# Performance work log

Hardware: AMD Instinct MI355X
Metric: run time of the kernel (lower is better)

Reference implementation:

```python
import jax, jax.numpy as jnp
import numpy as np

B, T, D, H = 8, 1024, 512, 8
D4 = 4 * D
SIGMA = 16.0
EPS = 1e-5


def layer_norm(x, w, b):
    m = jnp.mean(x, axis=-1, keepdims=True)
    v = jnp.mean((x - m) ** 2, axis=-1, keepdims=True)
    return (x - m) * jax.lax.rsqrt(v + EPS) * w + b


def setup_inputs() -> dict:
    key = jax.random.key(0)
    ks = jax.random.split(key, 12)
    return {
        "x": jax.random.normal(ks[0], (B, T, D), jnp.float32),
        "posv": jax.random.randint(ks[1], (B, T), 0, 64, jnp.int32),
        "posh": jax.random.randint(ks[2], (B, T), 0, 64, jnp.int32),
        "norm1_w": jnp.ones((D,), jnp.float32),
        "norm1_b": jnp.zeros((D,), jnp.float32),
        "in_w": jax.random.normal(ks[3], (3 * D, D), jnp.float32) * (D ** -0.5),
        "in_b": jnp.zeros((3 * D,), jnp.float32),
        "out_w": jax.random.normal(ks[4], (D, D), jnp.float32) * (D ** -0.5),
        "out_b": jnp.zeros((D,), jnp.float32),
        "norm2_w": jnp.ones((D,), jnp.float32),
        "norm2_b": jnp.zeros((D,), jnp.float32),
        "w1": jax.random.normal(ks[5], (D4, D), jnp.float32) * (D ** -0.5),
        "b1": jnp.zeros((D4,), jnp.float32),
        "w2": jax.random.normal(ks[6], (D, D4), jnp.float32) * (D4 ** -0.5),
        "b2": jnp.zeros((D,), jnp.float32),
        "gate": jnp.array(0.0, jnp.float32),
    }


def reference(x, posv, posh, norm1_w, norm1_b, in_w, in_b, out_w, out_b,
              norm2_w, norm2_b, w1, b1, w2, b2, gate):
    hd = D // H
    residual = x
    xn = layer_norm(x, norm1_w, norm1_b)

    # --- standard multi-head self-attention (dropout=eval identity) ---
    qkv = xn @ in_w.T + in_b                       # [B,T,3D]
    q, k, v = jnp.split(qkv, 3, axis=-1)
    q = q.reshape(B, T, H, hd).transpose(0, 2, 1, 3)  # [B,H,T,hd]
    k = k.reshape(B, T, H, hd).transpose(0, 2, 1, 3)
    v = v.reshape(B, T, H, hd).transpose(0, 2, 1, 3)
    scores = jnp.einsum("bhqd,bhkd->bhqk", q, k) * (hd ** -0.5)
    attn = jax.nn.softmax(scores, axis=-1)
    ctx = jnp.einsum("bhqk,bhkd->bhqd", attn, v)   # [B,H,T,hd]
    ctx = ctx.transpose(0, 2, 1, 3).reshape(B, T, D)
    std_out = ctx @ out_w.T + out_b

    # --- Gaussian kernel position attention ---
    pos = jnp.stack([posv, posh], axis=-1).astype(jnp.float32)  # [B,T,2]
    dist_sq = jnp.sum((pos[:, :, None, :] - pos[:, None, :, :]) ** 2, axis=-1)  # [B,T,T]
    kw = jnp.exp(-dist_sq / (2.0 * SIGMA ** 2))
    kw = kw / jnp.sum(kw, axis=-1, keepdims=True)
    kernel_out = kw @ xn                            # [B,T,D]

    g = jax.nn.sigmoid(gate)
    x1 = residual + g * std_out + (1.0 - g) * kernel_out

    # --- MLP block ---
    xn2 = layer_norm(x1, norm2_w, norm2_b)
    h = jax.nn.gelu(xn2 @ w1.T + b1, approximate=False)
    return x1 + h @ w2.T + b2
```

## Files before the change

### kernel.cpp

```cpp
#include <hip/hip_runtime.h>
#include <hip/hip_bf16.h>
#include <math.h>

typedef unsigned short ushort_t;
typedef short short8 __attribute__((ext_vector_type(8)));
typedef float f32x4 __attribute__((ext_vector_type(4)));

__device__ __forceinline__ float b2f(ushort_t u) {
  union { unsigned u; float f; } v; v.u = ((unsigned)u) << 16; return v.f;
}
__device__ __forceinline__ ushort_t f2b(float f) {
  union { float f; unsigned u; } v; v.f = f;
  unsigned r = (v.u + 0x7FFFu + ((v.u >> 16) & 1u)) >> 16;
  return (ushort_t)r;
}
__device__ __forceinline__ float gelu_fast(float v) {
  float u = 0.7978845608f * (v + 0.044715f * v * v * v);
  float a = fabsf(u);
  float t = exp2f(a * -2.8853900817779268f);
  float th = (1.f - t) / (1.f + t);
  th = copysignf(th, u);
  return 0.5f * v * (1.f + th);
}

union U16x8 { uint4 v; ushort_t s[8]; };

typedef const __attribute__((address_space(1))) unsigned int glb_u32;
typedef __attribute__((address_space(3))) unsigned int lds_u32;
__device__ __forceinline__ void gl_lds16(const ushort_t* g, ushort_t* l) {
  __builtin_amdgcn_global_load_lds((glb_u32*)g, (lds_u32*)l, 16, 0, 0);
}

__global__ __launch_bounds__(256) void cvt4_kernel(const float* __restrict__ s0,
                                                   const float* __restrict__ s1,
                                                   const float* __restrict__ s2,
                                                   const float* __restrict__ s3,
                                                   ushort_t* __restrict__ d0,
                                                   ushort_t* __restrict__ d1,
                                                   ushort_t* __restrict__ d2,
                                                   ushort_t* __restrict__ d3) {
  long i = (long)blockIdx.x * 256 + threadIdx.x;
  const float* s; ushort_t* d; long off;
  if (i < 196608)       { s = s0; d = d0; off = i; }
  else if (i < 262144)  { s = s1; d = d1; off = i - 196608; }
  else if (i < 524288)  { s = s2; d = d2; off = i - 262144; }
  else                  { s = s3; d = d3; off = i - 524288; }
  float4 f = *(const float4*)(s + off * 4);
  union { uint2 v; ushort_t s[4]; } o;
  o.s[0] = f2b(f.x); o.s[1] = f2b(f.y); o.s[2] = f2b(f.z); o.s[3] = f2b(f.w);
  *(uint2*)(d + off * 4) = o.v;
}

__global__ __launch_bounds__(256) void ln_kernel(const float* __restrict__ x,
                                                 const float* __restrict__ w,
                                                 const float* __restrict__ b,
                                                 ushort_t* __restrict__ out) {
  int tid = threadIdx.x, wave = tid >> 6, lane = tid & 63;
  long token = (long)blockIdx.x * 4 + wave;
  const float* xr = x + token * 512 + lane * 8;
  float4 a0 = *(const float4*)xr;
  float4 a1 = *(const float4*)(xr + 4);
  float xf[8] = {a0.x, a0.y, a0.z, a0.w, a1.x, a1.y, a1.z, a1.w};
  float s = 0.f, sq = 0.f;
#pragma unroll
  for (int i = 0; i < 8; i++) { s += xf[i]; sq += xf[i] * xf[i]; }
#pragma unroll
  for (int off = 1; off < 64; off <<= 1) { s += __shfl_xor(s, off); sq += __shfl_xor(sq, off); }
  float m = s * (1.f / 512.f);
  float var = sq * (1.f / 512.f) - m * m;
  float rs = rsqrtf(var + 1e-5f);
  float4 w0 = *(const float4*)(w + lane * 8);
  float4 w1v = *(const float4*)(w + lane * 8 + 4);
  float4 b0 = *(const float4*)(b + lane * 8);
  float4 b1v = *(const float4*)(b + lane * 8 + 4);
  float wf[8] = {w0.x, w0.y, w0.z, w0.w, w1v.x, w1v.y, w1v.z, w1v.w};
  float bf[8] = {b0.x, b0.y, b0.z, b0.w, b1v.x, b1v.y, b1v.z, b1v.w};
  U16x8 o;
#pragma unroll
  for (int i = 0; i < 8; i++) o.s[i] = f2b((xf[i] - m) * rs * wf[i] + bf[i]);
  *(uint4*)(out + token * 512 + lane * 8) = o.v;
}

__global__ __launch_bounds__(256) void ln_b_kernel(const ushort_t* __restrict__ x,
                                                   const float* __restrict__ w,
                                                   const float* __restrict__ b,
                                                   ushort_t* __restrict__ out) {
  int tid = threadIdx.x, wave = tid >> 6, lane = tid & 63;
  long token = (long)blockIdx.x * 4 + wave;
  U16x8 ux; ux.v = *(const uint4*)(x + token * 512 + lane * 8);
  float xf[8], s = 0.f, sq = 0.f;
#pragma unroll
  for (int i = 0; i < 8; i++) { xf[i] = b2f(ux.s[i]); s += xf[i]; sq += xf[i] * xf[i]; }
#pragma unroll
  for (int off = 1; off < 64; off <<= 1) { s += __shfl_xor(s, off); sq += __shfl_xor(sq, off); }
  float m = s * (1.f / 512.f);
  float var = sq * (1.f / 512.f) - m * m;
  float rs = rsqrtf(var + 1e-5f);
  float4 w0 = *(const float4*)(w + lane * 8);
  float4 w1v = *(const float4*)(w + lane * 8 + 4);
  float4 b0 = *(const float4*)(b + lane * 8);
  float4 b1v = *(const float4*)(b + lane * 8 + 4);
  float wf[8] = {w0.x, w0.y, w0.z, w0.w, w1v.x, w1v.y, w1v.z, w1v.w};
  float bf[8] = {b0.x, b0.y, b0.z, b0.w, b1v.x, b1v.y, b1v.z, b1v.w};
  U16x8 o;
#pragma unroll
  for (int i = 0; i < 8; i++) o.s[i] = f2b((xf[i] - m) * rs * wf[i] + bf[i]);
  *(uint4*)(out + token * 512 + lane * 8) = o.v;
}

__global__ __launch_bounds__(256) void kw_kernel(const int* __restrict__ posv,
                                                 const int* __restrict__ posh,
                                                 ushort_t* __restrict__ kw) {
  int b = blockIdx.x >> 10, i = blockIdx.x & 1023;
  int tid = threadIdx.x;
  const int* pv = posv + b * 1024;
  const int* ph = posh + b * 1024;
  int pvi = pv[i], phi = ph[i];
  int j0 = tid * 4;
  int4 vj = *(const int4*)(pv + j0);
  int4 hj = *(const int4*)(ph + j0);
  int vv[4] = {vj.x, vj.y, vj.z, vj.w};
  int hh[4] = {hj.x, hj.y, hj.z, hj.w};
  float e[4]; float loc = 0.f;
#pragma unroll
  for (int u = 0; u < 4; u++) {
    int dv = pvi - vv[u], dh = phi - hh[u];
    e[u] = expf((float)(dv * dv + dh * dh) * (-1.f / 512.f));
    loc += e[u];
  }
#pragma unroll
  for (int off = 1; off < 64; off <<= 1) loc += __shfl_xor(loc, off);
  __shared__ float wsum[4];
  __shared__ float tot;
  if ((tid & 63) == 0) wsum[tid >> 6] = loc;
  __syncthreads();
  if (tid == 0) tot = wsum[0] + wsum[1] + wsum[2] + wsum[3];
  __syncthreads();
  float inv = 1.f / tot;
  union { uint2 v; ushort_t s[4]; } o;
#pragma unroll
  for (int u = 0; u < 4; u++) o.s[u] = f2b(e[u] * inv);
  *(uint2*)&kw[((long)(b * 1024 + i)) * 1024 + j0] = o.v;
}

__global__ __launch_bounds__(256) void tr_kernel(const ushort_t* __restrict__ in,
                                                 ushort_t* __restrict__ out,
                                                 int R, int C) {
  __shared__ ushort_t tile[64 * 64];
  int z = blockIdx.z, r0 = blockIdx.y * 64, c0 = blockIdx.x * 64;
  const ushort_t* src = in + (long)z * R * C;
  ushort_t* dst = out + (long)z * R * C;
  int tid = threadIdx.x;
  int tr = tid >> 2;
  const ushort_t* s = src + (long)(r0 + tr) * C + c0;
  int g = (tr + (tr >> 4)) & 7;
#pragma unroll
  for (int u = 0; u < 2; u++) {
    int c = (tid & 3) + u * 4;
    *(uint4*)&tile[tr * 64 + (c ^ g) * 8] = *(const uint4*)(s + c * 8);
  }
  __syncthreads();
  int oc = tid >> 2, ob = (tid & 3) * 16;
  U16x8 o0, o1;
#pragma unroll
  for (int j = 0; j < 16; j++) {
    int r = ob + j;
    int gg = (r + (r >> 4)) & 7;
    ushort_t val = tile[r * 64 + (((oc >> 3) ^ gg)) * 8 + (oc & 7)];
    if (j < 8) o0.s[j] = val; else o1.s[j - 8] = val;
  }
  ushort_t* d = dst + (long)(c0 + oc) * R + r0 + ob;
  *(uint4*)d = o0.v;
  *(uint4*)(d + 8) = o1.v;
}

struct GemmP {
  const ushort_t* A; const ushort_t* Bm;
  long sA, sB, sC;
  int lda, ldb, ldc, K;
  const float* biasf;
  const float* residf;
  const ushort_t* auxb;
  const float* auxf;
  float* outf;
  ushort_t* outb;
  ushort_t* qp; ushort_t* kp; ushort_t* vp;
  const float* gate;
};

template <int BM, int BN, int EPI>
__global__ __launch_bounds__(256) void gemm_k(GemmP p) {
  constexpr int TI = BM / 32, TJ = BN / 32;
  constexpr int RA = BM / 64, RB = BN / 64;
  __shared__ ushort_t As[4][BM * 32];
  __shared__ ushort_t Bs[4][BN * 32];
  int tid = threadIdx.x, wv = tid >> 6, lane = tid & 63;
  int quad = lane >> 4, l15 = lane & 15;
  int bl = blockIdx.x + gridDim.x * blockIdx.y;
  int m0 = (bl % gridDim.y) * BM;
  int n0 = (bl / gridDim.y) * BN;
  int z = blockIdx.z;
  const ushort_t* A = p.A + (long)z * p.sA;
  const ushort_t* Bm = p.Bm + (long)z * p.sB;
  int wm = (wv & 1) * (BM / 2), wn = (wv >> 1) * (BN / 2);
  f32x4 acc[TI][TJ];
#pragma unroll
  for (int i = 0; i < TI; i++)
#pragma unroll
    for (int j = 0; j < TJ; j++)
#pragma unroll
      for (int r = 0; r < 4; r++) acc[i][j][r] = 0.f;

  int srow = tid >> 2;
  int sc = ((tid & 3) ^ ((tid >> 3) & 3)) * 8;
  const ushort_t* ga = A + (long)(m0 + srow) * p.lda + sc;
  const ushort_t* gb = Bm + (long)(n0 + srow) * p.ldb + sc;
  long a64 = (long)64 * p.lda, b64 = (long)64 * p.ldb;
  int aswz = (quad ^ ((l15 >> 1) & 3)) * 8;
  int nsteps = p.K >> 5;

#pragma unroll
  for (int s = 0; s < 2; s++) {
#pragma unroll
    for (int rr = 0; rr < RA; rr++)
      gl_lds16(ga + s * 32 + rr * a64, As[s] + rr * 2048 + wv * 512);
#pragma unroll
    for (int rr = 0; rr < RB; rr++)
      gl_lds16(gb + s * 32 + rr * b64, Bs[s] + rr * 2048 + wv * 512);
  }
  __syncthreads();

  for (int ks = 0; ks < nsteps; ks += 2) {
    if (ks + 2 < nsteps) {
#pragma unroll
      for (int s = 0; s < 2; s++) {
        int st = ks + 2 + s, bf = st & 3;
        const ushort_t* a0 = ga + st * 32;
        const ushort_t* b0 = gb + st * 32;
#pragma unroll
        for (int rr = 0; rr < RA; rr++)
          gl_lds16(a0 + rr * a64, As[bf] + rr * 2048 + wv * 512);
#pragma unroll
        for (int rr = 0; rr < RB; rr++)
          gl_lds16(b0 + rr * b64, Bs[bf] + rr * 2048 + wv * 512);
      }
    }
#pragma unroll
    for (int hs = 0; hs < 2; hs++) {
      int cur = (ks + hs) & 3;
      short8 av[TI], bv[TJ];
#pragma unroll
      for (int ti = 0; ti < TI; ti++)
        av[ti] = *(const short8*)&As[cur][(wm + ti * 16 + l15) * 32 + aswz];
#pragma unroll
      for (int tj = 0; tj < TJ; tj++)
        bv[tj] = *(const short8*)&Bs[cur][(wn + tj * 16 + l15) * 32 + aswz];
#pragma unroll
      for (int ti = 0; ti < TI; ti++)
#pragma unroll
        for (int tj = 0; tj < TJ; tj++)
          acc[ti][tj] = __builtin_amdgcn_mfma_f32_16x16x32_bf16(av[ti], bv[tj], acc[ti][tj], 0, 0, 0);
    }
    __syncthreads();
  }

  float g = 0.f;
  if constexpr (EPI == 2) g = 1.f / (1.f + expf(-p.gate[0]));
#pragma unroll
  for (int ti = 0; ti < TI; ti++) {
#pragma unroll
    for (int tj = 0; tj < TJ; tj++) {
#pragma unroll
      for (int r = 0; r < 4; r++) {
        int gm = m0 + wm + ti * 16 + quad * 4 + r;
        int n = n0 + wn + tj * 16 + l15;
        float v = acc[ti][tj][r];
        if constexpr (EPI == 0) {
          v += p.biasf[n];
          int bb = gm >> 10, tt = gm & 1023;
          if (n < 512) {
            int h = n >> 6, d = n & 63;
            p.qp[((long)(bb * 8 + h) * 1024 + tt) * 64 + d] = f2b(v * 0.18033688011112042f);
          } else if (n < 1024) {
            int n2 = n - 512, h = n2 >> 6, d = n2 & 63;
            p.kp[((long)(bb * 8 + h) * 1024 + tt) * 64 + d] = f2b(v);
          } else {
            int n2 = n - 1024, h = n2 >> 6, d = n2 & 63;
            p.vp[((long)(bb * 8 + h) * 1024 + tt) * 64 + d] = f2b(v);
          }
        } else if constexpr (EPI == 1) {
          p.outb[(long)z * p.sC + (long)gm * p.ldc + n] = f2b(v);
        } else if constexpr (EPI == 2) {
          v += p.biasf[n];
          long idx = (long)gm * 512 + n;
          p.outb[idx] = f2b(p.residf[idx] + g * v + (1.f - g) * b2f(p.auxb[idx]));
        } else if constexpr (EPI == 3) {
          v += p.biasf[n];
          p.outb[(long)gm * p.ldc + n] = f2b(gelu_fast(v));
        } else {
          v += p.biasf[n];
          long idx = (long)gm * 512 + n;
          p.outf[idx] = v + b2f(p.auxb[idx]);
        }
      }
    }
  }
}

template <int EPI>
__global__ __launch_bounds__(512, 2) void gemm256_k(GemmP p) {
  __shared__ __align__(16) ushort_t As[2][256 * 64];
  __shared__ __align__(16) ushort_t Bs[2][256 * 64];
  int tid = threadIdx.x, wv = tid >> 6, lane = tid & 63;
  int quad = lane >> 4, l15 = lane & 15;
  int m0 = blockIdx.x * 256, n0 = blockIdx.y * 256;
  int wr = wv >> 2, wc = wv & 3;

  int srow = tid >> 3;
  int scol = ((tid & 7) ^ (srow & 7)) * 8;
  const ushort_t* ga = p.A + (long)(m0 + srow) * p.lda + scol;
  const ushort_t* gb = p.Bm + (long)(n0 + srow) * p.ldb + scol;
  long a64 = (long)64 * p.lda, b64 = (long)64 * p.ldb;
  int NT = p.K >> 6;

  f32x4 acc[8][4];
#pragma unroll
  for (int i = 0; i < 8; i++)
#pragma unroll
    for (int j = 0; j < 4; j++)
#pragma unroll
      for (int r = 0; r < 4; r++) acc[i][j][r] = 0.f;

  gl_lds16(gb + 0 * b64, Bs[0] + 0 * 4096 + wv * 512);
  gl_lds16(gb + 1 * b64, Bs[0] + 1 * 4096 + wv * 512);
  gl_lds16(gb + 2 * b64, Bs[0] + 2 * 4096 + wv * 512);
  gl_lds16(gb + 3 * b64, Bs[0] + 3 * 4096 + wv * 512);
  gl_lds16(ga + 0 * a64, As[0] + 0 * 4096 + wv * 512);
  gl_lds16(ga + 2 * a64, As[0] + 2 * 4096 + wv * 512);
  gl_lds16(ga + 1 * a64, As[0] + 1 * 4096 + wv * 512);
  gl_lds16(ga + 3 * a64, As[0] + 3 * 4096 + wv * 512);
  asm volatile("s_waitcnt vmcnt(2)" ::: "memory");
  __builtin_amdgcn_s_barrier();

  int c0 = (quad ^ (l15 & 7)) * 8;
  int c1 = ((quad + 4) ^ (l15 & 7)) * 8;

  for (int t = 0; t < NT; t++) {
    int bt = t & 1, nx = bt ^ 1;
    bool pre = (t + 1 < NT);
    const ushort_t* Ab = &As[bt][(wr * 128 + l15) * 64];
    const ushort_t* Bb = &Bs[bt][(wc * 64 + l15) * 64];
    const ushort_t* gak = ga + (t + 1) * 64;
    const ushort_t* gbk = gb + (t + 1) * 64;
    short8 a[8], bn0[4], bn1[4];

#pragma unroll
    for (int mf = 0; mf < 4; mf++) {
      a[2 * mf]     = *(const short8*)(Ab + mf * 1024 + c0);
      a[2 * mf + 1] = *(const short8*)(Ab + mf * 1024 + c1);
    }
#pragma unroll
    for (int nf = 0; nf < 2; nf++) {
      bn0[2 * nf]     = *(const short8*)(Bb + nf * 1024 + c0);
      bn0[2 * nf + 1] = *(const short8*)(Bb + nf * 1024 + c1);
    }
    if (pre) {
      gl_lds16(gbk + 0 * b64, Bs[nx] + 0 * 4096 + wv * 512);
      gl_lds16(gbk + 1 * b64, Bs[nx] + 1 * 4096 + wv * 512);
    }
    __builtin_amdgcn_s_barrier();
    __builtin_amdgcn_s_setprio(1);
#pragma unroll
    for (int mf = 0; mf < 4; mf++)
#pragma unroll
      for (int nf = 0; nf < 2; nf++) {
        acc[mf][nf] = __builtin_amdgcn_mfma_f32_16x16x32_bf16(a[2 * mf], bn0[2 * nf], acc[mf][nf], 0, 0, 0);
        acc[mf][nf] = __builtin_amdgcn_mfma_f32_16x16x32_bf16(a[2 * mf + 1], bn0[2 * nf + 1], acc[mf][nf], 0, 0, 0);
      }
    __builtin_amdgcn_s_setprio(0);
    __builtin_amdgcn_s_barrier();

#pragma unroll
    for (int nf = 0; nf < 2; nf++) {
      bn1[2 * nf]     = *(const short8*)(Bb + (2 + nf) * 1024 + c0);
      bn1[2 * nf + 1] = *(const short8*)(Bb + (2 + nf) * 1024 + c1);
    }
    if (pre) {
      gl_lds16(gbk + 2 * b64, Bs[nx] + 2 * 4096 + wv * 512);
      gl_lds16(gbk + 3 * b64, Bs[nx] + 3 * 4096 + wv * 512);
    }
    __builtin_amdgcn_s_barrier();
    __builtin_amdgcn_s_setprio(1);
#pragma unroll
    for (int mf = 0; mf < 4; mf++)
#pragma unroll
      for (int nf = 0; nf < 2; nf++) {
        acc[mf][2 + nf] = __builtin_amdgcn_mfma_f32_16x16x32_bf16(a[2 * mf], bn1[2 * nf], acc[mf][2 + nf], 0, 0, 0);
        acc[mf][2 + nf] = __builtin_amdgcn_mfma_f32_16x16x32_bf16(a[2 * mf + 1], bn1[2 * nf + 1], acc[mf][2 + nf], 0, 0, 0);
      }
    __builtin_amdgcn_s_setprio(0);
    if (pre) asm volatile("s_waitcnt vmcnt(4)" ::: "memory");
    else     asm volatile("s_waitcnt vmcnt(0)" ::: "memory");
    __builtin_amdgcn_s_barrier();

#pragma unroll
    for (int mf = 0; mf < 4; mf++) {
      a[2 * mf]     = *(const short8*)(Ab + (4 + mf) * 1024 + c0);
      a[2 * mf + 1] = *(const short8*)(Ab + (4 + mf) * 1024 + c1);
    }
    if (pre) {
      gl_lds16(gak + 0 * a64, As[nx] + 0 * 4096 + wv * 512);
      gl_lds16(gak + 2 * a64, As[nx] + 2 * 4096 + wv * 512);
    }
    __builtin_amdgcn_s_barrier();
    __builtin_amdgcn_s_setprio(1);
#pragma unroll
    for (int mf = 0; mf < 4; mf++)
#pragma unroll
      for (int nf = 0; nf < 2; nf++) {
        acc[4 + mf][2 + nf] = __builtin_amdgcn_mfma_f32_16x16x32_bf16(a[2 * mf], bn1[2 * nf], acc[4 + mf][2 + nf], 0, 0, 0);
        acc[4 + mf][2 + nf] = __builtin_amdgcn_mfma_f32_16x16x32_bf16(a[2 * mf + 1], bn1[2 * nf + 1], acc[4 + mf][2 + nf], 0, 0, 0);
      }
    __builtin_amdgcn_s_setprio(0);
    __builtin_amdgcn_s_barrier();

    if (pre) {
      gl_lds16(gak + 1 * a64, As[nx] + 1 * 4096 + wv * 512);
      gl_lds16(gak + 3 * a64, As[nx] + 3 * 4096 + wv * 512);
    }
    __builtin_amdgcn_s_barrier();
    __builtin_amdgcn_s_setprio(1);
#pragma unroll
    for (int mf = 0; mf < 4; mf++)
#pragma unroll
      for (int nf = 0; nf < 2; nf++) {
        acc[4 + mf][nf] = __builtin_amdgcn_mfma_f32_16x16x32_bf16(a[2 * mf], bn0[2 * nf], acc[4 + mf][nf], 0, 0, 0);
        acc[4 + mf][nf] = __builtin_amdgcn_mfma_f32_16x16x32_bf16(a[2 * mf + 1], bn0[2 * nf + 1], acc[4 + mf][nf], 0, 0, 0);
      }
    __builtin_amdgcn_s_setprio(0);
    if (pre) asm volatile("s_waitcnt vmcnt(2)" ::: "memory");
    __builtin_amdgcn_s_barrier();
  }

#pragma unroll
  for (int mf = 0; mf < 8; mf++) {
#pragma unroll
    for (int nf = 0; nf < 4; nf++) {
#pragma unroll
      for (int r = 0; r < 4; r++) {
        int gm = m0 + wr * 128 + mf * 16 + quad * 4 + r;
        int n = n0 + wc * 64 + nf * 16 + l15;
        float v = acc[mf][nf][r];
        if constexpr (EPI == 0) {
          v += p.biasf[n];
          int bb = gm >> 10, tt = gm & 1023;
          if (n < 512) {
            int h = n >> 6, d = n & 63;
            p.qp[((long)(bb * 8 + h) * 1024 + tt) * 64 + d] = f2b(v * 0.18033688011112042f);
          } else if (n < 1024) {
            int n2 = n - 512, h = n2 >> 6, d = n2 & 63;
            p.kp[((long)(bb * 8 + h) * 1024 + tt) * 64 + d] = f2b(v);
          } else {
            int n2 = n - 1024, h = n2 >> 6, d = n2 & 63;
            p.vp[((long)(bb * 8 + h) * 1024 + tt) * 64 + d] = f2b(v);
          }
        } else {
          v += p.biasf[n];
          p.outb[(long)gm * p.ldc + n] = f2b(gelu_fast(v));
        }
      }
    }
  }
}

__global__ __launch_bounds__(256) void flash_k(const ushort_t* __restrict__ q,
                                               const ushort_t* __restrict__ k,
                                               const ushort_t* __restrict__ vT,
                                               ushort_t* __restrict__ ctx) {
  int bl = blockIdx.x + gridDim.x * blockIdx.y;
  int bh = bl % 64;
  int q0 = (bl / 64) * 128;
  int tid = threadIdx.x, wv = tid >> 6, lane = tid & 63;
  int quad = lane >> 4, l15 = lane & 15;
  __shared__ ushort_t Ks[2][64 * 64], Vt[2][64 * 64];
  __shared__ ushort_t Pt[128 * 64];
  int wm = wv * 32;

  short8 qf[2][2];
#pragma unroll
  for (int tq = 0; tq < 2; tq++)
#pragma unroll
    for (int kk = 0; kk < 2; kk++)
      qf[tq][kk] = *(const short8*)&q[((long)bh * 1024 + q0 + wm + tq * 16 + l15) * 64 + kk * 32 + quad * 8];

  int srow = tid >> 3;
  int sc = ((tid & 7) ^ ((tid >> 3) & 7)) * 8;
#pragma unroll
  for (int e = 0; e < 2; e++) {
    gl_lds16(&k[((long)bh * 1024 + e * 32 + srow) * 64 + sc], Ks[0] + e * 2048 + wv * 512);
    gl_lds16(&vT[((long)bh * 64 + e * 32 + srow) * 1024 + sc], Vt[0] + e * 2048 + wv * 512);
  }
  __syncthreads();

  f32x4 O[2][4];
#pragma unroll
  for (int tq = 0; tq < 2; tq++)
#pragma unroll
    for (int td = 0; td < 4; td++)
#pragma unroll
      for (int r = 0; r < 4; r++) O[tq][td][r] = 0.f;
  float ls[2] = {0.f, 0.f};

  int pswz = (l15 & 7) << 1;
  for (int kt = 0; kt < 16; kt++) {
    int cur = kt & 1;
    if (kt + 1 < 16) {
#pragma unroll
      for (int e = 0; e < 2; e++) {
        gl_lds16(&k[((long)bh * 1024 + (kt + 1) * 64 + e * 32 + srow) * 64 + sc], Ks[cur ^ 1] + e * 2048 + wv * 512);
        gl_lds16(&vT[((long)bh * 64 + e * 32 + srow) * 1024 + (kt + 1) * 64 + sc], Vt[cur ^ 1] + e * 2048 + wv * 512);
      }
    }
#pragma unroll
    for (int tq = 0; tq < 2; tq++) {
      f32x4 S[4];
#pragma unroll
      for (int tk = 0; tk < 4; tk++) {
#pragma unroll
        for (int r = 0; r < 4; r++) S[tk][r] = 0.f;
#pragma unroll
        for (int kk = 0; kk < 2; kk++) {
          short8 kf = *(const short8*)&Ks[cur][(tk * 16 + l15) * 64 + ((kk * 4 + quad) ^ (l15 & 7)) * 8];
          S[tk] = __builtin_amdgcn_mfma_f32_16x16x32_bf16(kf, qf[tq][kk], S[tk], 0, 0, 0);
        }
      }
#pragma unroll
      for (int tk = 0; tk < 4; tk++) {
        float p0 = exp2f(S[tk][0]);
        float p1 = exp2f(S[tk][1]);
        float p2 = exp2f(S[tk][2]);
        float p3 = exp2f(S[tk][3]);
        ls[tq] += (p0 + p1) + (p2 + p3);
        unsigned lo = __builtin_amdgcn_perm(__float_as_uint(p1), __float_as_uint(p0), 0x07060302u);
        unsigned hi = __builtin_amdgcn_perm(__float_as_uint(p3), __float_as_uint(p2), 0x07060302u);
        int gnum = (tk * 4 + quad) ^ pswz;
        uint2 pr; pr.x = lo; pr.y = hi;
        *(uint2*)&Pt[(wm + tq * 16 + l15) * 64 + gnum * 4] = pr;
      }
    }
#pragma unroll
    for (int tq = 0; tq < 2; tq++) {
#pragma unroll
      for (int kk = 0; kk < 2; kk++) {
        short8 pf = *(const short8*)&Pt[(wm + tq * 16 + l15) * 64 + (((kk * 8 + quad * 2) ^ pswz)) * 4];
#pragma unroll
        for (int td = 0; td < 4; td++) {
          short8 vf = *(const short8*)&Vt[cur][(td * 16 + l15) * 64 + ((kk * 4 + quad) ^ (l15 & 7)) * 8];
          O[tq][td] = __builtin_amdgcn_mfma_f32_16x16x32_bf16(pf, vf, O[tq][td], 0, 0, 0);
        }
      }
    }
    __syncthreads();
  }
#pragma unroll
  for (int tq = 0; tq < 2; tq++) {
    ls[tq] += __shfl_xor(ls[tq], 16);
    ls[tq] += __shfl_xor(ls[tq], 32);
  }
  int bb = bh >> 3, h = bh & 7;
#pragma unroll
  for (int tq = 0; tq < 2; tq++) {
#pragma unroll
    for (int r = 0; r < 4; r++) {
      int qrow = quad * 4 + r;
      float inv = 1.f / __shfl(ls[tq], (lane & 48) | qrow);
      long row = (long)bb * 1024 + q0 + wm + tq * 16 + qrow;
#pragma unroll
      for (int td = 0; td < 4; td++)
        ctx[row * 512 + h * 64 + td * 16 + l15] = f2b(O[tq][td][r] * inv);
    }
  }
}

extern "C" void kernel_launch(void* const* d_in, const int* in_sizes, int n_in,
                              void* d_out, int out_size, void* d_ws, size_t ws_size,
                              hipStream_t stream) {
  const float* x    = (const float*)d_in[0];
  const int* posv   = (const int*)d_in[1];
  const int* posh   = (const int*)d_in[2];
  const float* n1w  = (const float*)d_in[3];
  const float* n1b  = (const float*)d_in[4];
  const float* in_w = (const float*)d_in[5];
  const float* in_b = (const float*)d_in[6];
  const float* outw = (const float*)d_in[7];
  const float* outb = (const float*)d_in[8];
  const float* n2w  = (const float*)d_in[9];
  const float* n2b  = (const float*)d_in[10];
  const float* w1   = (const float*)d_in[11];
  const float* b1   = (const float*)d_in[12];
  const float* w2   = (const float*)d_in[13];
  const float* b2   = (const float*)d_in[14];
  const float* gate = (const float*)d_in[15];
  float* out = (float*)d_out;

  char* ws = (char*)d_ws;
  const size_t MB = 1024 * 1024;
  ushort_t* q    = (ushort_t*)(ws + 0 * MB);
  ushort_t* kk   = (ushort_t*)(ws + 8 * MB);
  ushort_t* vtmp = (ushort_t*)(ws + 16 * MB);
  ushort_t* vT   = (ushort_t*)(ws + 24 * MB);
  ushort_t* kw   = (ushort_t*)(ws + 32 * MB);
  ushort_t* xn   = (ushort_t*)(ws + 48 * MB);
  ushort_t* xnT  = (ushort_t*)(ws + 56 * MB);
  ushort_t* ctx  = (ushort_t*)(ws + 64 * MB);
  ushort_t* ko   = (ushort_t*)(ws + 72 * MB);
  ushort_t* x1b  = (ushort_t*)(ws + 80 * MB);
  ushort_t* xn2  = (ushort_t*)(ws + 16 * MB);
  ushort_t* inwb = (ushort_t*)(ws + 96 * MB);
  ushort_t* owb  = (ushort_t*)(ws + 98 * MB);
  ushort_t* w1b  = (ushort_t*)(ws + 99 * MB);
  ushort_t* w2b  = (ushort_t*)(ws + 101 * MB);
  ushort_t* h    = (ushort_t*)(ws + 24 * MB);

  cvt4_kernel<<<3072, 256, 0, stream>>>(in_w, outw, w1, w2, inwb, owb, w1b, w2b);
  ln_kernel<<<2048, 256, 0, stream>>>(x, n1w, n1b, xn);
  kw_kernel<<<8192, 256, 0, stream>>>(posv, posh, kw);
  {
    GemmP p = {};
    p.A = xn; p.Bm = inwb; p.lda = 512; p.ldb = 512; p.K = 512;
    p.biasf = in_b; p.qp = q; p.kp = kk; p.vp = vtmp;
    gemm256_k<0><<<dim3(32, 6), 512, 0, stream>>>(p);
  }
  tr_kernel<<<dim3(1, 16, 64), 256, 0, stream>>>(vtmp, vT, 1024, 64);
  flash_k<<<dim3(8, 64, 1), 256, 0, stream>>>(q, kk, vT, ctx);
  tr_kernel<<<dim3(8, 16, 8), 256, 0, stream>>>(xn, xnT, 1024, 512);
  {
    GemmP p = {};
    p.A = kw; p.Bm = xnT; p.lda = 1024; p.ldb = 1024; p.ldc = 512; p.K = 1024;
    p.sA = 1024L * 1024; p.sB = 512L * 1024; p.sC = 1024L * 512;
    p.outb = ko;
    gemm_k<64, 128, 1><<<dim3(4, 16, 8), 256, 0, stream>>>(p);
  }
  {
    GemmP p = {};
    p.A = ctx; p.Bm = owb; p.lda = 512; p.ldb = 512; p.K = 512;
    p.biasf = outb; p.residf = x; p.auxb = ko; p.outb = x1b; p.gate = gate;
    gemm_k<64, 64, 2><<<dim3(8, 128, 1), 256, 0, stream>>>(p);
  }
  ln_b_kernel<<<2048, 256, 0, stream>>>(x1b, n2w, n2b, xn2);
  {
    GemmP p = {};
    p.A = xn2; p.Bm = w1b; p.lda = 512; p.ldb = 512; p.ldc = 2048; p.K = 512;
    p.biasf = b1; p.outb = h;
    gemm256_k<3><<<dim3(32, 8), 512, 0, stream>>>(p);
  }
  {
    GemmP p = {};
    p.A = h; p.Bm = w2b; p.lda = 2048; p.ldb = 2048; p.K = 2048;
    p.biasf = b2; p.auxb = x1b; p.outf = out;
    gemm_k<64, 128, 4><<<dim3(4, 128, 1), 256, 0, stream>>>(p);
  }
}
```

Baseline: 290.9 us.

## Fuse Gaussian kernel-weight generation into the kernel-attention GEMM

Drops the separate kw_kernel that wrote a full B×T×T bf16 weight matrix to global memory. The new GEMM kernel computes the unnormalized Gaussian weights on the fly from the position arrays while staging its A tiles into shared memory, accumulates row sums, and normalizes in the epilogue. This removes a 16MB write and the matching read, plus one launch. In exchange, each output-column block recomputes the exponentials redundantly (4x across N tiles) and normalizes after rounding to bf16, so numerics shift slightly.

Result: no change. 295.9 us (+1.7%).

```diff
diff --git a/kernel.cpp b/kernel.cpp
--- a/kernel.cpp
+++ b/kernel.cpp
@@ -106,41 +106,6 @@
 #pragma unroll
   for (int i = 0; i < 8; i++) o.s[i] = f2b((xf[i] - m) * rs * wf[i] + bf[i]);
   *(uint4*)(out + token * 512 + lane * 8) = o.v;
-}
-
-__global__ __launch_bounds__(256) void kw_kernel(const int* __restrict__ posv,
-                                                 const int* __restrict__ posh,
-                                                 ushort_t* __restrict__ kw) {
-  int b = blockIdx.x >> 10, i = blockIdx.x & 1023;
-  int tid = threadIdx.x;
-  const int* pv = posv + b * 1024;
-  const int* ph = posh + b * 1024;
-  int pvi = pv[i], phi = ph[i];
-  int j0 = tid * 4;
-  int4 vj = *(const int4*)(pv + j0);
-  int4 hj = *(const int4*)(ph + j0);
-  int vv[4] = {vj.x, vj.y, vj.z, vj.w};
-  int hh[4] = {hj.x, hj.y, hj.z, hj.w};
-  float e[4]; float loc = 0.f;
-#pragma unroll
-  for (int u = 0; u < 4; u++) {
-    int dv = pvi - vv[u], dh = phi - hh[u];
-    e[u] = expf((float)(dv * dv + dh * dh) * (-1.f / 512.f));
-    loc += e[u];
-  }
-#pragma unroll
-  for (int off = 1; off < 64; off <<= 1) loc += __shfl_xor(loc, off);
-  __shared__ float wsum[4];
-  __shared__ float tot;
-  if ((tid & 63) == 0) wsum[tid >> 6] = loc;
-  __syncthreads();
-  if (tid == 0) tot = wsum[0] + wsum[1] + wsum[2] + wsum[3];
-  __syncthreads();
-  float inv = 1.f / tot;
-  union { uint2 v; ushort_t s[4]; } o;
-#pragma unroll
-  for (int u = 0; u < 4; u++) o.s[u] = f2b(e[u] * inv);
-  *(uint2*)&kw[((long)(b * 1024 + i)) * 1024 + j0] = o.v;
 }
 
 __global__ __launch_bounds__(256) void tr_kernel(const ushort_t* __restrict__ in,
@@ -307,6 +272,118 @@
   }
 }
 
+__global__ __launch_bounds__(256) void gemm_kw_k(const int* __restrict__ posv,
+                                                 const int* __restrict__ posh,
+                                                 const ushort_t* __restrict__ xnT,
+                                                 ushort_t* __restrict__ ko) {
+  constexpr int BM = 64, BN = 128, TI = 2, TJ = 4, RB = 2, NSTEPS = 32;
+  __shared__ ushort_t As[4][BM * 32];
+  __shared__ ushort_t Bs[4][BN * 32];
+  __shared__ float rsm[64];
+  int tid = threadIdx.x, wv = tid >> 6, lane = tid & 63;
+  int quad = lane >> 4, l15 = lane & 15;
+  int bl = blockIdx.x + gridDim.x * blockIdx.y;
+  int m0 = (bl % gridDim.y) * BM;
+  int n0 = (bl / gridDim.y) * BN;
+  int z = blockIdx.z;
+  const int* pv = posv + z * 1024;
+  const int* ph = posh + z * 1024;
+  const ushort_t* Bm = xnT + (long)z * 512 * 1024;
+  int wm = (wv & 1) * 32, wn = (wv >> 1) * 64;
+  f32x4 acc[TI][TJ];
+#pragma unroll
+  for (int i = 0; i < TI; i++)
+#pragma unroll
+    for (int j = 0; j < TJ; j++)
+#pragma unroll
+      for (int r = 0; r < 4; r++) acc[i][j][r] = 0.f;
+
+  int srow = tid >> 2;
+  int sc = ((tid & 3) ^ ((tid >> 3) & 3)) * 8;
+  const ushort_t* gb = Bm + (long)(n0 + srow) * 1024 + sc;
+  long b64 = (long)64 * 1024;
+  int aswz = (quad ^ ((l15 >> 1) & 3)) * 8;
+  int pvi = pv[m0 + srow], phi = ph[m0 + srow];
+  float rsum = 0.f;
+
+#define STAGE_A(st, bf)                                                        \
+  {                                                                            \
+    int j0 = (st) * 32 + sc;                                                   \
+    int4 v0 = *(const int4*)(pv + j0); int4 v1 = *(const int4*)(pv + j0 + 4);  \
+    int4 h0 = *(const int4*)(ph + j0); int4 h1 = *(const int4*)(ph + j0 + 4);  \
+    int vv[8] = {v0.x, v0.y, v0.z, v0.w, v1.x, v1.y, v1.z, v1.w};              \
+    int hh[8] = {h0.x, h0.y, h0.z, h0.w, h1.x, h1.y, h1.z, h1.w};              \
+    U16x8 o;                                                                   \
+    _Pragma("unroll")                                                          \
+    for (int u = 0; u < 8; u++) {                                              \
+      int dv = pvi - vv[u], dh = phi - hh[u];                                  \
+      float e = exp2f((float)(dv * dv + dh * dh) * -0.0028177637517362566f);   \
+      rsum += e; o.s[u] = f2b(e);                                              \
+    }                                                                          \
+    *(uint4*)&As[bf][tid * 8] = o.v;                                           \
+  }
+
+#pragma unroll
+  for (int s = 0; s < 2; s++) {
+    STAGE_A(s, s);
+#pragma unroll
+    for (int rr = 0; rr < RB; rr++)
+      gl_lds16(gb + s * 32 + rr * b64, Bs[s] + rr * 2048 + wv * 512);
+  }
+  __syncthreads();
+
+  for (int ks = 0; ks < NSTEPS; ks += 2) {
+    if (ks + 2 < NSTEPS) {
+#pragma unroll
+      for (int s = 0; s < 2; s++) {
+        int st = ks + 2 + s, bf = st & 3;
+        STAGE_A(st, bf);
+        const ushort_t* b0 = gb + st * 32;
+#pragma unroll
+        for (int rr = 0; rr < RB; rr++)
+          gl_lds16(b0 + rr * b64, Bs[bf] + rr * 2048 + wv * 512);
+      }
+    }
+#pragma unroll
+    for (int hs = 0; hs < 2; hs++) {
+      int cur = (ks + hs) & 3;
+      short8 av[TI], bv[TJ];
+#pragma unroll
+      for (int ti = 0; ti < TI; ti++)
+        av[ti] = *(const short8*)&As[cur][(wm + ti * 16 + l15) * 32 + aswz];
+#pragma unroll
+      for (int tj = 0; tj < TJ; tj++)
+        bv[tj] = *(const short8*)&Bs[cur][(wn + tj * 16 + l15) * 32 + aswz];
+#pragma unroll
+      for (int ti = 0; ti < TI; ti++)
+#pragma unroll
+        for (int tj = 0; tj < TJ; tj++)
+          acc[ti][tj] = __builtin_amdgcn_mfma_f32_16x16x32_bf16(av[ti], bv[tj], acc[ti][tj], 0, 0, 0);
+    }
+    __syncthreads();
+  }
+#undef STAGE_A
+
+  rsum += __shfl_xor(rsum, 1);
+  rsum += __shfl_xor(rsum, 2);
+  if ((tid & 3) == 0) rsm[srow] = rsum;
+  __syncthreads();
+
+#pragma unroll
+  for (int ti = 0; ti < TI; ti++) {
+#pragma unroll
+    for (int r = 0; r < 4; r++) {
+      int lr = wm + ti * 16 + quad * 4 + r;
+      float inv = 1.f / rsm[lr];
+#pragma unroll
+      for (int tj = 0; tj < TJ; tj++) {
+        int n = n0 + wn + tj * 16 + l15;
+        ko[(long)z * 1024 * 512 + (long)(m0 + lr) * 512 + n] = f2b(acc[ti][tj][r] * inv);
+      }
+    }
+  }
+}
+
 template <int EPI>
 __global__ __launch_bounds__(512, 2) void gemm256_k(GemmP p) {
   __shared__ __align__(16) ushort_t As[2][256 * 64];
@@ -609,7 +686,6 @@
   ushort_t* kk   = (ushort_t*)(ws + 8 * MB);
   ushort_t* vtmp = (ushort_t*)(ws + 16 * MB);
   ushort_t* vT   = (ushort_t*)(ws + 24 * MB);
-  ushort_t* kw   = (ushort_t*)(ws + 32 * MB);
   ushort_t* xn   = (ushort_t*)(ws + 48 * MB);
   ushort_t* xnT  = (ushort_t*)(ws + 56 * MB);
   ushort_t* ctx  = (ushort_t*)(ws + 64 * MB);
@@ -624,7 +700,6 @@
 
   cvt4_kernel<<<3072, 256, 0, stream>>>(in_w, outw, w1, w2, inwb, owb, w1b, w2b);
   ln_kernel<<<2048, 256, 0, stream>>>(x, n1w, n1b, xn);
-  kw_kernel<<<8192, 256, 0, stream>>>(posv, posh, kw);
   {
     GemmP p = {};
     p.A = xn; p.Bm = inwb; p.lda = 512; p.ldb = 512; p.K = 512;
@@ -634,13 +709,7 @@
   tr_kernel<<<dim3(1, 16, 64), 256, 0, stream>>>(vtmp, vT, 1024, 64);
   flash_k<<<dim3(8, 64, 1), 256, 0, stream>>>(q, kk, vT, ctx);
   tr_kernel<<<dim3(8, 16, 8), 256, 0, stream>>>(xn, xnT, 1024, 512);
-  {
-    GemmP p = {};
-    p.A = kw; p.Bm = xnT; p.lda = 1024; p.ldb = 1024; p.ldc = 512; p.K = 1024;
-    p.sA = 1024L * 1024; p.sB = 512L * 1024; p.sC = 1024L * 512;
-    p.outb = ko;
-    gemm_k<64, 128, 1><<<dim3(4, 16, 8), 256, 0, stream>>>(p);
-  }
+  gemm_kw_k<<<dim3(4, 16, 8), 256, 0, stream>>>(posv, posh, xnT, ko);
   {
     GemmP p = {};
     p.A = ctx; p.Bm = owb; p.lda = 512; p.ldb = 512; p.K = 512;
```
